# Performance work log

Measured on AMD Instinct MI355X. Metric: run time of the kernel, lower is better.

The kernel has to match this reference:

```python
import jax, jax.numpy as jnp
import numpy as np

DIM = 1024
HEADS = 16
HEAD_DIM = DIM // HEADS
SCALE = HEAD_DIM ** -0.5


def setup_inputs() -> dict:
    key = jax.random.key(0)
    ks = jax.random.split(key, 7)
    B, N, M = 2, 2048, 2048
    x = jax.random.normal(ks[0], (B, N, DIM), dtype=jnp.float32)
    y = jax.random.normal(ks[1], (B, M, DIM), dtype=jnp.float32)
    s = DIM ** -0.5
    Wq = jax.random.normal(ks[2], (DIM, DIM), dtype=jnp.float32) * s
    Wk = jax.random.normal(ks[3], (DIM, DIM), dtype=jnp.float32) * s
    Wv = jax.random.normal(ks[4], (DIM, DIM), dtype=jnp.float32) * s
    Wp = jax.random.normal(ks[5], (DIM, DIM), dtype=jnp.float32) * s
    bp = jax.random.normal(ks[6], (DIM,), dtype=jnp.float32) * 0.01
    return {"x": x, "y": y, "Wq": Wq, "Wk": Wk, "Wv": Wv, "Wp": Wp, "bp": bp}


def _split_heads(t):
    b, n, _ = t.shape
    return t.reshape(b, n, HEADS, HEAD_DIM).transpose(0, 2, 1, 3)  # b h n d


def reference(x, y, Wq, Wk, Wv, Wp, bp):
    q = _split_heads(x @ Wq)  # [b,h,n,d]
    k = _split_heads(y @ Wk)  # [b,h,m,d]
    v = _split_heads(y @ Wv)  # [b,h,m,d]
    attn = jnp.einsum('bhid,bhjd->bhij', q, k) * SCALE  # [b,h,n,m]
    attn = jax.nn.softmax(attn, axis=-1)
    out = jnp.einsum('bhij,bhjd->bhid', attn, v)  # [b,h,n,d]
    b, h, n, d = out.shape
    out = out.transpose(0, 2, 1, 3).reshape(b, n, h * d)  # [b,n,dim]
    return out @ Wp + bp
```

## Files before the change

### kernel.cpp

```cpp
#include <hip/hip_runtime.h>
#include <hip/hip_bf16.h>
#include <cstdint>

#define DIM   1024
#define HEADS 16
#define HDIM  64
#define BATCH 2
#define SEQ   2048
#define ROWS  (BATCH*SEQ)
static constexpr float QSCALE = 0.18033688f;

typedef float  f32x4  __attribute__((ext_vector_type(4)));
typedef float  float4v __attribute__((ext_vector_type(4)));
typedef __bf16 bf16x8 __attribute__((ext_vector_type(8)));
typedef __bf16 bf16x4 __attribute__((ext_vector_type(4)));
typedef short  short4v __attribute__((ext_vector_type(4)));

#if __has_builtin(__builtin_amdgcn_mfma_f32_16x16x16_bf16)
__device__ __forceinline__ f32x4 mfma16(bf16x4 a, bf16x4 b, f32x4 c) {
  return __builtin_amdgcn_mfma_f32_16x16x16_bf16(a, b, c, 0, 0, 0);
}
#else
__device__ __forceinline__ f32x4 mfma16(bf16x4 a, bf16x4 b, f32x4 c) {
  return __builtin_amdgcn_mfma_f32_16x16x16bf16_1k(
      __builtin_bit_cast(short4v, a), __builtin_bit_cast(short4v, b), c, 0, 0, 0);
}
#endif

__device__ __forceinline__ void glds16(const __bf16* g, __bf16* l) {
  __builtin_amdgcn_global_load_lds(
      (const __attribute__((address_space(1))) void*)g,
      (__attribute__((address_space(3))) void*)l, 16, 0, 0);
}

__global__ __launch_bounds__(256) void prep_kernel(
    const float* __restrict__ x, const float* __restrict__ y,
    const float* __restrict__ Wq, const float* __restrict__ Wk,
    const float* __restrict__ Wv, const float* __restrict__ Wp,
    __bf16* __restrict__ xb, __bf16* __restrict__ yb, __bf16* __restrict__ Wt) {
  const int z = blockIdx.z, t = threadIdx.x;
  const size_t NEL = (size_t)ROWS * DIM;
  if (z < 8) {
    size_t idx = (((size_t)z * 1024 + blockIdx.x) * 256 + t) * 4;
    const float* s; __bf16* d;
    if (idx < NEL) { s = x + idx; d = xb + idx; }
    else           { s = y + (idx - NEL); d = yb + (idx - NEL); }
    const float4v v = *(const float4v*)s;
    bf16x4 o;
    o[0] = (__bf16)v[0]; o[1] = (__bf16)v[1]; o[2] = (__bf16)v[2]; o[3] = (__bf16)v[3];
    *(bf16x4*)d = o;
    return;
  }
  const int w = blockIdx.x >> 8, rem = blockIdx.x & 255;
  const float* W = (w == 0) ? Wq : (w == 1) ? Wk : (w == 2) ? Wv : Wp;
  __bf16* dst = Wt + (size_t)w * DIM * DIM;
  const int n0 = (rem & 15) * 64, k0 = (rem >> 4) * 64;
  __shared__ float T[64][65];
  const int col = t & 63, rw = t >> 6;
  #pragma unroll
  for (int p = 0; p < 16; ++p) {
    const int row = p * 4 + rw;
    T[row][col] = W[(size_t)(k0 + row) * DIM + n0 + col];
  }
  __syncthreads();
  #pragma unroll
  for (int p = 0; p < 16; ++p) {
    const int row = p * 4 + rw;
    dst[(size_t)(n0 + row) * DIM + k0 + col] = (__bf16)T[col][row];
  }
}

__global__ __launch_bounds__(256) void proj_kernel(
    const __bf16* __restrict__ xb, const __bf16* __restrict__ yb,
    const __bf16* __restrict__ Wt,
    __bf16* __restrict__ Qb, __bf16* __restrict__ Kb, __bf16* __restrict__ VT) {
  const int z = blockIdx.z;
  const __bf16* A = (z == 0) ? xb : yb;
  const __bf16* B = Wt + (size_t)z * DIM * DIM;

  __shared__ __bf16 As[128 * 64];
  __shared__ __bf16 Bs[128 * 64];

  const int t = threadIdx.x, lane = t & 63, wave = t >> 6;
  const int l15 = lane & 15, quad = lane >> 4;
  const int wm = wave & 1, wn = wave >> 1;
  const int rowBase = blockIdx.y * 128, colBase = blockIdx.x * 128;
  const int srow = lane >> 3;
  const int scol = ((lane & 7) ^ srow) * 8;

  f32x4 acc[4][4] = {};

  for (int kb = 0; kb < DIM; kb += 64) {
    __syncthreads();
    #pragma unroll
    for (int i = 0; i < 4; ++i) {
      const int c = wave * 4 + i;
      const int row = c * 8 + srow;
      glds16(&A[(size_t)(rowBase + row) * DIM + kb + scol], &As[c * 512]);
      glds16(&B[(size_t)(colBase + row) * DIM + kb + scol], &Bs[c * 512]);
    }
    __syncthreads();
    #pragma unroll
    for (int ks = 0; ks < 2; ++ks) {
      bf16x8 a[4], b[4];
      #pragma unroll
      for (int mi = 0; mi < 4; ++mi) {
        const int row = wm * 64 + mi * 16 + l15;
        a[mi] = *(const bf16x8*)&As[row * 64 + (((ks << 2) | quad) ^ (row & 7)) * 8];
      }
      #pragma unroll
      for (int ni = 0; ni < 4; ++ni) {
        const int row = wn * 64 + ni * 16 + l15;
        b[ni] = *(const bf16x8*)&Bs[row * 64 + (((ks << 2) | quad) ^ (row & 7)) * 8];
      }
      #pragma unroll
      for (int mi = 0; mi < 4; ++mi)
        #pragma unroll
        for (int ni = 0; ni < 4; ++ni)
          acc[mi][ni] = __builtin_amdgcn_mfma_f32_16x16x32_bf16(a[mi], b[ni], acc[mi][ni], 0, 0, 0);
    }
  }

  if (z < 2) {
    __bf16* out = (z == 0) ? Qb : Kb;
    const float sc = (z == 0) ? QSCALE : 1.0f;
    #pragma unroll
    for (int mi = 0; mi < 4; ++mi) {
      const int row0 = rowBase + wm * 64 + mi * 16 + quad * 4;
      #pragma unroll
      for (int ni = 0; ni < 4; ++ni) {
        const int col = colBase + wn * 64 + ni * 16 + l15;
        #pragma unroll
        for (int r = 0; r < 4; ++r)
          out[(size_t)(row0 + r) * DIM + col] = (__bf16)(acc[mi][ni][r] * sc);
      }
    }
  } else {
    #pragma unroll
    for (int mi = 0; mi < 4; ++mi) {
      const int row0 = rowBase + wm * 64 + mi * 16 + quad * 4;
      const int bb = row0 >> 11, key0 = row0 & (SEQ - 1);
      #pragma unroll
      for (int ni = 0; ni < 4; ++ni) {
        const int col = colBase + wn * 64 + ni * 16 + l15;
        const int h = col >> 6, d = col & 63;
        bf16x4 pk;
        #pragma unroll
        for (int r = 0; r < 4; ++r) pk[r] = (__bf16)acc[mi][ni][r];
        *(bf16x4*)&VT[((size_t)((bb * HEADS + h) * HDIM + d)) * SEQ + key0] = pk;
      }
    }
  }
}

__global__ __launch_bounds__(256, 2) void attn_kernel(
    const __bf16* __restrict__ Qb, const __bf16* __restrict__ Kb,
    const __bf16* __restrict__ VT, __bf16* __restrict__ Ob) {
  __shared__ __bf16 KV[2][2][64 * 64];
  __shared__ float lb[2][128];

  const int t = threadIdx.x, lane = t & 63, wave = t >> 6;
  const int l15 = lane & 15, quad = lane >> 4;
  const int bh = blockIdx.y, b = bh >> 4, h = bh & 15;
  const int qseg = wave & 1, kh = wave >> 1;
  const int qrow0 = blockIdx.x * 128 + qseg * 64;
  const int srow = lane >> 3;
  const int scol = ((lane & 7) ^ srow) * 8;

  const __bf16* Kbh = Kb + (size_t)b * SEQ * DIM + h * HDIM;
  const __bf16* Vbh = VT + (size_t)bh * HDIM * SEQ;

  bf16x8 qf[4][2];
  #pragma unroll
  for (int mi = 0; mi < 4; ++mi)
    #pragma unroll
    for (int ks = 0; ks < 2; ++ks)
      qf[mi][ks] = *(const bf16x8*)&Qb[(size_t)(b * SEQ + qrow0 + mi * 16 + l15) * DIM
                                       + h * HDIM + ks * 32 + quad * 8];

  f32x4 o[4][4] = {};
  float lsum[4] = {};

  auto stage = [&](int jb, int buf) {
    #pragma unroll
    for (int i = 0; i < 2; ++i) {
      const int c = wave * 2 + i;
      const int row = c * 8 + srow;
      glds16(&Kbh[(size_t)(jb + row) * DIM + scol], &KV[buf][0][c * 512]);
      glds16(&Vbh[(size_t)row * SEQ + jb + scol], &KV[buf][1][c * 512]);
    }
  };

  stage(0, 0);
  for (int j = 0; j < SEQ / 64; ++j) {
    const int buf = j & 1;
    __syncthreads();
    if (j + 1 < SEQ / 64) stage((j + 1) * 64, buf ^ 1);
    const __bf16* Ks = KV[buf][0];
    const __bf16* Vs = KV[buf][1];

    f32x4 sT[2][4] = {};
    #pragma unroll
    for (int ks = 0; ks < 2; ++ks)
      #pragma unroll
      for (int ni = 0; ni < 2; ++ni) {
        const int key = kh * 32 + ni * 16 + l15;
        const bf16x8 kf = *(const bf16x8*)&Ks[key * 64 + (((ks << 2) | quad) ^ (key & 7)) * 8];
        #pragma unroll
        for (int mi = 0; mi < 4; ++mi)
          sT[ni][mi] = __builtin_amdgcn_mfma_f32_16x16x32_bf16(kf, qf[mi][ks], sT[ni][mi], 0, 0, 0);
      }

    bf16x4 pa[2][4];
    #pragma unroll
    for (int ni = 0; ni < 2; ++ni)
      #pragma unroll
      for (int mi = 0; mi < 4; ++mi)
        #pragma unroll
        for (int r = 0; r < 4; ++r) {
          const float pv = __builtin_amdgcn_exp2f(sT[ni][mi][r]);
          lsum[mi] += pv;
          pa[ni][mi][r] = (__bf16)pv;
        }

    #pragma unroll
    for (int ni = 0; ni < 2; ++ni) {
      const int key0 = kh * 32 + ni * 16;
      #pragma unroll
      for (int dt = 0; dt < 4; ++dt) {
        const int d = dt * 16 + l15;
        const bf16x4 vf = *(const bf16x4*)&Vs[d * 64
            + (((key0 >> 3) + (quad >> 1)) ^ (d & 7)) * 8 + (quad & 1) * 4];
        #pragma unroll
        for (int mi = 0; mi < 4; ++mi)
          o[mi][dt] = mfma16(pa[ni][mi], vf, o[mi][dt]);
      }
    }
  }

  #pragma unroll
  for (int mi = 0; mi < 4; ++mi) {
    lsum[mi] += __shfl_xor(lsum[mi], 16, 64);
    lsum[mi] += __shfl_xor(lsum[mi], 32, 64);
  }
  __syncthreads();
  float* mb = (float*)&KV[0][0][0];
  if (quad == 0) {
    #pragma unroll
    for (int mi = 0; mi < 4; ++mi)
      lb[kh][qseg * 64 + mi * 16 + l15] = lsum[mi];
  }
  if (kh == 1) {
    #pragma unroll
    for (int mi = 0; mi < 4; ++mi)
      #pragma unroll
      for (int r = 0; r < 4; ++r) {
        const int q = mi * 16 + quad * 4 + r;
        #pragma unroll
        for (int dt = 0; dt < 4; ++dt)
          mb[qseg * 4096 + q * 64 + dt * 16 + l15] = o[mi][dt][r];
      }
  }
  __syncthreads();
  if (kh == 0) {
    #pragma unroll
    for (int mi = 0; mi < 4; ++mi)
      #pragma unroll
      for (int r = 0; r < 4; ++r) {
        const int q = mi * 16 + quad * 4 + r;
        const float inv = 1.f / (lb[0][qseg * 64 + q] + lb[1][qseg * 64 + q]);
        const size_t row = (size_t)(b * SEQ + qrow0 + q);
        #pragma unroll
        for (int dt = 0; dt < 4; ++dt) {
          const float ov = o[mi][dt][r] + mb[qseg * 4096 + q * 64 + dt * 16 + l15];
          Ob[row * DIM + h * HDIM + dt * 16 + l15] = (__bf16)(ov * inv);
        }
      }
  }
}

__global__ __launch_bounds__(256) void outproj_kernel(
    const __bf16* __restrict__ A, const __bf16* __restrict__ Bt,
    const float* __restrict__ bias, float* __restrict__ out) {
  __shared__ __bf16 As[128 * 64];
  __shared__ __bf16 Bs[128 * 64];

  const int t = threadIdx.x, lane = t & 63, wave = t >> 6;
  const int l15 = lane & 15, quad = lane >> 4;
  const int wm = wave & 1, wn = wave >> 1;
  const int rowBase = blockIdx.y * 128, colBase = blockIdx.x * 128;
  const int srow = lane >> 3;
  const int scol = ((lane & 7) ^ srow) * 8;

  f32x4 acc[4][4] = {};

  for (int kb = 0; kb < DIM; kb += 64) {
    __syncthreads();
    #pragma unroll
    for (int i = 0; i < 4; ++i) {
      const int c = wave * 4 + i;
      const int row = c * 8 + srow;
      glds16(&A[(size_t)(rowBase + row) * DIM + kb + scol], &As[c * 512]);
      glds16(&Bt[(size_t)(colBase + row) * DIM + kb + scol], &Bs[c * 512]);
    }
    __syncthreads();
    #pragma unroll
    for (int ks = 0; ks < 2; ++ks) {
      bf16x8 a[4], b[4];
      #pragma unroll
      for (int mi = 0; mi < 4; ++mi) {
        const int row = wm * 64 + mi * 16 + l15;
        a[mi] = *(const bf16x8*)&As[row * 64 + (((ks << 2) | quad) ^ (row & 7)) * 8];
      }
      #pragma unroll
      for (int ni = 0; ni < 4; ++ni) {
        const int row = wn * 64 + ni * 16 + l15;
        b[ni] = *(const bf16x8*)&Bs[row * 64 + (((ks << 2) | quad) ^ (row & 7)) * 8];
      }
      #pragma unroll
      for (int mi = 0; mi < 4; ++mi)
        #pragma unroll
        for (int ni = 0; ni < 4; ++ni)
          acc[mi][ni] = __builtin_amdgcn_mfma_f32_16x16x32_bf16(a[mi], b[ni], acc[mi][ni], 0, 0, 0);
    }
  }

  #pragma unroll
  for (int mi = 0; mi < 4; ++mi) {
    const int row0 = rowBase + wm * 64 + mi * 16 + quad * 4;
    #pragma unroll
    for (int ni = 0; ni < 4; ++ni) {
      const int col = colBase + wn * 64 + ni * 16 + l15;
      const float bb = bias[col];
      #pragma unroll
      for (int r = 0; r < 4; ++r)
        out[(size_t)(row0 + r) * DIM + col] = acc[mi][ni][r] + bb;
    }
  }
}

extern "C" void kernel_launch(void* const* d_in, const int* in_sizes, int n_in,
                              void* d_out, int out_size, void* d_ws, size_t ws_size,
                              hipStream_t stream) {
  const float* x  = (const float*)d_in[0];
  const float* y  = (const float*)d_in[1];
  const float* Wq = (const float*)d_in[2];
  const float* Wk = (const float*)d_in[3];
  const float* Wv = (const float*)d_in[4];
  const float* Wp = (const float*)d_in[5];
  const float* bp = (const float*)d_in[6];
  float* out = (float*)d_out;

  const size_t NEL = (size_t)ROWS * DIM;
  __bf16* xb = (__bf16*)d_ws;
  __bf16* yb = xb + NEL;
  __bf16* Wt = yb + NEL;
  __bf16* Qb = Wt + NEL;
  __bf16* Kb = Qb + NEL;
  __bf16* VT = Kb + NEL;
  __bf16* Ob = VT + NEL;

  prep_kernel<<<dim3(1024, 1, 9), 256, 0, stream>>>(x, y, Wq, Wk, Wv, Wp, xb, yb, Wt);
  proj_kernel<<<dim3(DIM / 128, ROWS / 128, 3), 256, 0, stream>>>(xb, yb, Wt, Qb, Kb, VT);
  attn_kernel<<<dim3(SEQ / 128, BATCH * HEADS), 256, 0, stream>>>(Qb, Kb, VT, Ob);
  outproj_kernel<<<dim3(DIM / 128, ROWS / 128), 256, 0, stream>>>(Ob, Wt + 3 * (size_t)DIM * DIM, bp, out);
}
```

Measured before the change: 214.1 us.

## Stage V transpose via LDS, MFMA row sums, smaller outproj tiles, reuse workspace

The V projection epilogue now writes its tile into shared memory with a swizzle, then stores coalesced 16-byte rows of the transposed V instead of scattered 8-byte writes. The attention kernel computes softmax denominators with an MFMA against a ones vector, replacing per-element adds and cross-lane shuffles. The output projection switches to 64-row tiles, doubling the block count for better CU occupancy. The attention output buffer now aliases the xb workspace. These changes trade extra LDS traffic and syncs, plus extra MFMA work, for fewer uncoalesced stores and less VALU work.

Result: no change. 212.4 us (-0.8%).

```diff
diff --git a/kernel.cpp b/kernel.cpp
--- a/kernel.cpp
+++ b/kernel.cpp
@@ -76,10 +76,11 @@
     __bf16* __restrict__ Qb, __bf16* __restrict__ Kb, __bf16* __restrict__ VT) {
   const int z = blockIdx.z;
   const __bf16* A = (z == 0) ? xb : yb;
-  const __bf16* B = Wt + (size_t)z * DIM * DIM;
-
-  __shared__ __bf16 As[128 * 64];
-  __shared__ __bf16 Bs[128 * 64];
+  const __bf16* Bt = Wt + (size_t)z * DIM * DIM;
+
+  __shared__ __bf16 S[2][128 * 64];
+  __bf16* As = S[0];
+  __bf16* Bs = S[1];
 
   const int t = threadIdx.x, lane = t & 63, wave = t >> 6;
   const int l15 = lane & 15, quad = lane >> 4;
@@ -97,7 +98,7 @@
       const int c = wave * 4 + i;
       const int row = c * 8 + srow;
       glds16(&A[(size_t)(rowBase + row) * DIM + kb + scol], &As[c * 512]);
-      glds16(&B[(size_t)(colBase + row) * DIM + kb + scol], &Bs[c * 512]);
+      glds16(&Bt[(size_t)(colBase + row) * DIM + kb + scol], &Bs[c * 512]);
     }
     __syncthreads();
     #pragma unroll
@@ -135,21 +136,33 @@
           out[(size_t)(row0 + r) * DIM + col] = (__bf16)(acc[mi][ni][r] * sc);
       }
     }
-  } else {
-    #pragma unroll
-    for (int mi = 0; mi < 4; ++mi) {
-      const int row0 = rowBase + wm * 64 + mi * 16 + quad * 4;
-      const int bb = row0 >> 11, key0 = row0 & (SEQ - 1);
-      #pragma unroll
-      for (int ni = 0; ni < 4; ++ni) {
-        const int col = colBase + wn * 64 + ni * 16 + l15;
-        const int h = col >> 6, d = col & 63;
-        bf16x4 pk;
-        #pragma unroll
-        for (int r = 0; r < 4; ++r) pk[r] = (__bf16)acc[mi][ni][r];
-        *(bf16x4*)&VT[((size_t)((bb * HEADS + h) * HDIM + d)) * SEQ + key0] = pk;
-      }
-    }
+    return;
+  }
+
+  __syncthreads();
+  __bf16* Ts = &S[0][0];
+  #pragma unroll
+  for (int mi = 0; mi < 4; ++mi) {
+    const int bk3 = wm * 8 + mi * 2 + (quad >> 1);
+    #pragma unroll
+    for (int ni = 0; ni < 4; ++ni) {
+      const int dl = wn * 64 + ni * 16 + l15;
+      bf16x4 pk;
+      #pragma unroll
+      for (int r = 0; r < 4; ++r) pk[r] = (__bf16)acc[mi][ni][r];
+      *(bf16x4*)&Ts[dl * 128 + (bk3 ^ (dl & 7)) * 8 + (quad & 1) * 4] = pk;
+    }
+  }
+  __syncthreads();
+  const int d = t >> 1, khh = t & 1;
+  const size_t vrow = (size_t)((rowBase >> 11) * HEADS * HDIM) + colBase + d;
+  const int key0g = rowBase & (SEQ - 1);
+  #pragma unroll
+  for (int j = 0; j < 8; ++j) {
+    const int kc = khh * 8 + j;
+    const int lc = (kc & 8) | ((kc ^ d) & 7);
+    const bf16x8 v = *(const bf16x8*)&Ts[d * 128 + lc * 8];
+    *(bf16x8*)&VT[vrow * SEQ + key0g + kc * 8] = v;
   }
 }
 
@@ -178,8 +191,12 @@
       qf[mi][ks] = *(const bf16x8*)&Qb[(size_t)(b * SEQ + qrow0 + mi * 16 + l15) * DIM
                                        + h * HDIM + ks * 32 + quad * 8];
 
+  bf16x4 ones4;
+  #pragma unroll
+  for (int i = 0; i < 4; ++i) ones4[i] = (__bf16)1.0f;
+
   f32x4 o[4][4] = {};
-  float lsum[4] = {};
+  f32x4 lacc[4] = {};
 
   auto stage = [&](int jb, int buf) {
     #pragma unroll
@@ -217,15 +234,15 @@
       #pragma unroll
       for (int mi = 0; mi < 4; ++mi)
         #pragma unroll
-        for (int r = 0; r < 4; ++r) {
-          const float pv = __builtin_amdgcn_exp2f(sT[ni][mi][r]);
-          lsum[mi] += pv;
-          pa[ni][mi][r] = (__bf16)pv;
-        }
+        for (int r = 0; r < 4; ++r)
+          pa[ni][mi][r] = (__bf16)__builtin_amdgcn_exp2f(sT[ni][mi][r]);
 
     #pragma unroll
     for (int ni = 0; ni < 2; ++ni) {
       const int key0 = kh * 32 + ni * 16;
+      #pragma unroll
+      for (int mi = 0; mi < 4; ++mi)
+        lacc[mi] = mfma16(pa[ni][mi], ones4, lacc[mi]);
       #pragma unroll
       for (int dt = 0; dt < 4; ++dt) {
         const int d = dt * 16 + l15;
@@ -238,17 +255,14 @@
     }
   }
 
-  #pragma unroll
-  for (int mi = 0; mi < 4; ++mi) {
-    lsum[mi] += __shfl_xor(lsum[mi], 16, 64);
-    lsum[mi] += __shfl_xor(lsum[mi], 32, 64);
-  }
   __syncthreads();
   float* mb = (float*)&KV[0][0][0];
-  if (quad == 0) {
+  if (l15 == 0) {
     #pragma unroll
     for (int mi = 0; mi < 4; ++mi)
-      lb[kh][qseg * 64 + mi * 16 + l15] = lsum[mi];
+      #pragma unroll
+      for (int r = 0; r < 4; ++r)
+        lb[kh][qseg * 64 + mi * 16 + quad * 4 + r] = lacc[mi][r];
   }
   if (kh == 1) {
     #pragma unroll
@@ -282,34 +296,39 @@
 __global__ __launch_bounds__(256) void outproj_kernel(
     const __bf16* __restrict__ A, const __bf16* __restrict__ Bt,
     const float* __restrict__ bias, float* __restrict__ out) {
-  __shared__ __bf16 As[128 * 64];
+  __shared__ __bf16 As[64 * 64];
   __shared__ __bf16 Bs[128 * 64];
 
   const int t = threadIdx.x, lane = t & 63, wave = t >> 6;
   const int l15 = lane & 15, quad = lane >> 4;
   const int wm = wave & 1, wn = wave >> 1;
-  const int rowBase = blockIdx.y * 128, colBase = blockIdx.x * 128;
+  const int rowBase = blockIdx.y * 64, colBase = blockIdx.x * 128;
   const int srow = lane >> 3;
   const int scol = ((lane & 7) ^ srow) * 8;
 
-  f32x4 acc[4][4] = {};
+  f32x4 acc[2][4] = {};
 
   for (int kb = 0; kb < DIM; kb += 64) {
     __syncthreads();
+    #pragma unroll
+    for (int i = 0; i < 2; ++i) {
+      const int c = wave * 2 + i;
+      const int row = c * 8 + srow;
+      glds16(&A[(size_t)(rowBase + row) * DIM + kb + scol], &As[c * 512]);
+    }
     #pragma unroll
     for (int i = 0; i < 4; ++i) {
       const int c = wave * 4 + i;
       const int row = c * 8 + srow;
-      glds16(&A[(size_t)(rowBase + row) * DIM + kb + scol], &As[c * 512]);
       glds16(&Bt[(size_t)(colBase + row) * DIM + kb + scol], &Bs[c * 512]);
     }
     __syncthreads();
     #pragma unroll
     for (int ks = 0; ks < 2; ++ks) {
-      bf16x8 a[4], b[4];
-      #pragma unroll
-      for (int mi = 0; mi < 4; ++mi) {
-        const int row = wm * 64 + mi * 16 + l15;
+      bf16x8 a[2], b[4];
+      #pragma unroll
+      for (int mi = 0; mi < 2; ++mi) {
+        const int row = wm * 32 + mi * 16 + l15;
         a[mi] = *(const bf16x8*)&As[row * 64 + (((ks << 2) | quad) ^ (row & 7)) * 8];
       }
       #pragma unroll
@@ -318,7 +337,7 @@
         b[ni] = *(const bf16x8*)&Bs[row * 64 + (((ks << 2) | quad) ^ (row & 7)) * 8];
       }
       #pragma unroll
-      for (int mi = 0; mi < 4; ++mi)
+      for (int mi = 0; mi < 2; ++mi)
         #pragma unroll
         for (int ni = 0; ni < 4; ++ni)
           acc[mi][ni] = __builtin_amdgcn_mfma_f32_16x16x32_bf16(a[mi], b[ni], acc[mi][ni], 0, 0, 0);
@@ -326,8 +345,8 @@
   }
 
   #pragma unroll
-  for (int mi = 0; mi < 4; ++mi) {
-    const int row0 = rowBase + wm * 64 + mi * 16 + quad * 4;
+  for (int mi = 0; mi < 2; ++mi) {
+    const int row0 = rowBase + wm * 32 + mi * 16 + quad * 4;
     #pragma unroll
     for (int ni = 0; ni < 4; ++ni) {
       const int col = colBase + wn * 64 + ni * 16 + l15;
@@ -358,10 +377,10 @@
   __bf16* Qb = Wt + NEL;
   __bf16* Kb = Qb + NEL;
   __bf16* VT = Kb + NEL;
-  __bf16* Ob = VT + NEL;
+  __bf16* Ob = xb;
 
   prep_kernel<<<dim3(1024, 1, 9), 256, 0, stream>>>(x, y, Wq, Wk, Wv, Wp, xb, yb, Wt);
   proj_kernel<<<dim3(DIM / 128, ROWS / 128, 3), 256, 0, stream>>>(xb, yb, Wt, Qb, Kb, VT);
   attn_kernel<<<dim3(SEQ / 128, BATCH * HEADS), 256, 0, stream>>>(Qb, Kb, VT, Ob);
-  outproj_kernel<<<dim3(DIM / 128, ROWS / 128), 256, 0, stream>>>(Ob, Wt + 3 * (size_t)DIM * DIM, bp, out);
-}
+  outproj_kernel<<<dim3(DIM / 128, ROWS / 64), 256, 0, stream>>>(Ob, Wt + 3 * NEL / 4, bp, out);
+}
```
